# Kernel tuning notes

Measured on AMD Instinct MI355X. Metric: run time of the kernel, lower is better.

Reference implementation:

```python
import jax, jax.numpy as jnp
import numpy as np

TEMPERATURE = 1.0
TOP_K = 50
TOP_P = 0.95
NEG_INF = float('-inf')


def setup_inputs() -> dict:
    key = jax.random.key(0)
    k1, k2, k3, k4 = jax.random.split(key, 4)
    B, S, D, V = 32, 8, 1024, 50257
    psi_real = jax.random.normal(k1, (B, S, D), dtype=jnp.float32)
    psi_imag = jax.random.normal(k2, (B, S, D), dtype=jnp.float32)
    W_real = jax.random.normal(k3, (V, D), dtype=jnp.float32) * 0.02
    W_imag = jax.random.normal(k4, (V, D), dtype=jnp.float32) * 0.02
    bias = jnp.zeros((V,), dtype=jnp.float32)
    return {"psi_real": psi_real, "psi_imag": psi_imag, "W_real": W_real,
            "W_imag": W_imag, "bias": bias}


def _legacy_filter(logits, temperature, top_k, top_p):
    # temperature
    l = logits / max(temperature, 1e-8)
    # top-k: keep values >= k-th largest
    if 0 < top_k < l.shape[-1]:
        topk_vals = jax.lax.top_k(l, top_k)[0]          # [B,S,k]
        threshold = topk_vals[..., -1:]
        l = jnp.where(l < threshold, NEG_INF, l)
    # top-p (nucleus): mask tokens where exclusive cumulative prob >= p
    if top_p < 1.0:
        p = max(top_p, 1e-6)
        order = jnp.argsort(-l, axis=-1)                # descending
        sl = jnp.take_along_axis(l, order, axis=-1)
        sp = jax.nn.softmax(sl, axis=-1)
        cum = jnp.cumsum(sp, axis=-1)
        mask = (cum - sp) >= p                          # exclusive cumsum >= p
        mask = mask.at[..., 0].set(False)               # always keep top token
        sl = jnp.where(mask, NEG_INF, sl)
        inv = jnp.argsort(order, axis=-1)               # scatter back to original order
        l = jnp.take_along_axis(sl, inv, axis=-1)
    return l


def reference(psi_real, psi_imag, W_real, W_imag, bias):
    # logits = proj_real(psi.real) + proj_imag(psi.imag) + bias  -> [B,S,V]
    logits = (jnp.einsum('bsd,vd->bsv', psi_real, W_real)
              + jnp.einsum('bsd,vd->bsv', psi_imag, W_imag) + bias)
    sampling_logits = _legacy_filter(logits, TEMPERATURE, TOP_K, TOP_P)
    probs = jax.nn.softmax(sampling_logits, axis=-1)
    # multinomial(probs, 1) == categorical over filtered logits
    tokens = jax.random.categorical(jax.random.key(42), sampling_logits, axis=-1)
    log_probs = jax.nn.log_softmax(logits, axis=-1)
    return logits, tokens, probs, log_probs
```

## Files before the change

kernel.cpp:

```cpp
#include <hip/hip_runtime.h>
#include <stdint.h>
#include <math.h>

#define MM 256
#define KD 1024
#define K2 2048
#define VV 50257
#define NF4 (VV / 4)

static constexpr size_t OUT_TOKENS = (size_t)MM * VV;
static constexpr size_t OUT_PROBS  = OUT_TOKENS + MM;
static constexpr size_t OUT_LOGPR  = OUT_PROBS + (size_t)MM * VV;

#define WS_ABUF_BYTES (2u * 1024u * 1024u)

typedef __attribute__((ext_vector_type(8))) short bf16x8;
typedef __attribute__((ext_vector_type(4))) float f32x4;

__device__ __forceinline__ ushort f2bf(float x) {
  unsigned u = __float_as_uint(x);
  unsigned r = u + 0x7FFFu + ((u >> 16) & 1u);
  return (ushort)(r >> 16);
}
__device__ __forceinline__ float bf2f(ushort h) {
  return __uint_as_float(((unsigned)h) << 16);
}

__device__ __forceinline__ unsigned rotl32(unsigned x, int r) {
  return (x << r) | (x >> (32 - r));
}

__device__ __forceinline__ uint2 threefry2x32(unsigned k0, unsigned k1,
                                              unsigned x0, unsigned x1) {
  unsigned ks[3] = {k0, k1, k0 ^ k1 ^ 0x1BD11BDAu};
  const int rot[8] = {13, 15, 26, 6, 17, 29, 16, 24};
  x0 += ks[0]; x1 += ks[1];
  #pragma unroll
  for (int g = 0; g < 5; ++g) {
    const int base = (g & 1) ? 4 : 0;
    #pragma unroll
    for (int i = 0; i < 4; ++i) {
      x0 += x1;
      x1 = rotl32(x1, rot[base + i]);
      x1 ^= x0;
    }
    x0 += ks[(g + 1) % 3];
    x1 += ks[(g + 2) % 3] + (unsigned)(g + 1);
  }
  return make_uint2(x0, x1);
}

__device__ __forceinline__ float gumbel_at(unsigned flat) {
  uint2 r = threefry2x32(0u, 42u, 0u, flat);
  unsigned w = r.x ^ r.y;
  unsigned fb = (w >> 9) | 0x3F800000u;
  float f = __uint_as_float(fb) - 1.0f;
  const float tiny = 1.1754943508222875e-38f;
  float u = fmaxf(tiny, f + tiny);
  float t1 = (float)log((double)u);
  float t3 = (float)log((double)(-t1));
  return -t3;
}

__global__ __launch_bounds__(256)
void k_prep(const float* __restrict__ psi_r, const float* __restrict__ psi_i,
            ushort* __restrict__ a_buf) {
  int t = blockIdx.x * 256 + threadIdx.x;
  int lane = t & 63;
  int mb = (t >> 6) & 15;
  int s = t >> 10;
  int lr = lane & 15, lg = lane >> 4;
  int m = mb * 16 + lr;
  int kloc = (s & 31) * 32 + lg * 8;
  const float* __restrict__ src = (s < 32) ? psi_r : psi_i;
  float4 v0 = *reinterpret_cast<const float4*>(&src[m * KD + kloc]);
  float4 v1 = *reinterpret_cast<const float4*>(&src[m * KD + kloc + 4]);
  float in[8] = {v0.x, v0.y, v0.z, v0.w, v1.x, v1.y, v1.z, v1.w};
  ushort h[8], l[8];
  #pragma unroll
  for (int j = 0; j < 8; ++j) {
    h[j] = f2bf(in[j]);
    l[j] = f2bf(in[j] - bf2f(h[j]));
  }
  size_t base = ((size_t)(s * 16 + mb) * 2) * 512 + (size_t)lane * 8;
  #pragma unroll
  for (int j = 0; j < 8; ++j) {
    a_buf[base + j] = h[j];
    a_buf[base + 512 + j] = l[j];
  }
}

#define BN 64
#define BK 64
#define GT 256

__global__ __launch_bounds__(GT, 2)
void k_gemm(const uint4* __restrict__ a_buf,
            const float* __restrict__ Wr, const float* __restrict__ Wi,
            const float* __restrict__ bias, float* __restrict__ logits) {
  __shared__ ushort sBh[2][BN * BK];
  __shared__ ushort sBl[2][BN * BK];

  const int tid  = threadIdx.x;
  const int lane = tid & 63;
  const int wid  = tid >> 6;
  const int vb   = blockIdx.x * BN;
  const int lr = lane & 15;
  const int lg = lane >> 4;

  const int brow = tid >> 2;
  const int bcol = (tid & 3) << 4;
  const int gn   = vb + brow;
  const int eo0  = brow * BK + (bcol ^ ((brow & 7) << 3));
  const int eo1  = brow * BK + ((bcol + 8) ^ ((brow & 7) << 3));

  f32x4 acc[4][4];
  #pragma unroll
  for (int i = 0; i < 4; ++i)
    #pragma unroll
    for (int j = 0; j < 4; ++j)
      #pragma unroll
      for (int q = 0; q < 4; ++q) acc[i][j][q] = 0.f;

  float4 w0 = make_float4(0.f, 0.f, 0.f, 0.f), w1 = w0, w2 = w0, w3 = w0;
  if (gn < VV) {
    const float* p = &Wr[(size_t)gn * KD + bcol];
    w0 = *reinterpret_cast<const float4*>(p);
    w1 = *reinterpret_cast<const float4*>(p + 4);
    w2 = *reinterpret_cast<const float4*>(p + 8);
    w3 = *reinterpret_cast<const float4*>(p + 12);
  }

  int cur = 0;
  for (int s2 = 0; s2 < K2 / BK; ++s2) {
    uint4 vah[2][4], val[2][4];
    #pragma unroll
    for (int kq = 0; kq < 2; ++kq) {
      #pragma unroll
      for (int mi = 0; mi < 4; ++mi) {
        int chunk2 = (((s2 * 2 + kq) * 16) + wid * 4 + mi) * 2;
        vah[kq][mi] = a_buf[(size_t)chunk2 * 64 + lane];
        val[kq][mi] = a_buf[(size_t)(chunk2 + 1) * 64 + lane];
      }
    }
    {
      float in[16] = {w0.x, w0.y, w0.z, w0.w, w1.x, w1.y, w1.z, w1.w,
                      w2.x, w2.y, w2.z, w2.w, w3.x, w3.y, w3.z, w3.w};
      ushort h[16], l[16];
      #pragma unroll
      for (int j = 0; j < 16; ++j) {
        h[j] = f2bf(in[j]);
        l[j] = f2bf(in[j] - bf2f(h[j]));
      }
      *reinterpret_cast<uint4*>(&sBh[cur][eo0]) =
          make_uint4((unsigned)h[0] | ((unsigned)h[1] << 16),
                     (unsigned)h[2] | ((unsigned)h[3] << 16),
                     (unsigned)h[4] | ((unsigned)h[5] << 16),
                     (unsigned)h[6] | ((unsigned)h[7] << 16));
      *reinterpret_cast<uint4*>(&sBh[cur][eo1]) =
          make_uint4((unsigned)h[8] | ((unsigned)h[9] << 16),
                     (unsigned)h[10] | ((unsigned)h[11] << 16),
                     (unsigned)h[12] | ((unsigned)h[13] << 16),
                     (unsigned)h[14] | ((unsigned)h[15] << 16));
      *reinterpret_cast<uint4*>(&sBl[cur][eo0]) =
          make_uint4((unsigned)l[0] | ((unsigned)l[1] << 16),
                     (unsigned)l[2] | ((unsigned)l[3] << 16),
                     (unsigned)l[4] | ((unsigned)l[5] << 16),
                     (unsigned)l[6] | ((unsigned)l[7] << 16));
      *reinterpret_cast<uint4*>(&sBl[cur][eo1]) =
          make_uint4((unsigned)l[8] | ((unsigned)l[9] << 16),
                     (unsigned)l[10] | ((unsigned)l[11] << 16),
                     (unsigned)l[12] | ((unsigned)l[13] << 16),
                     (unsigned)l[14] | ((unsigned)l[15] << 16));
    }
    if (s2 < K2 / BK - 1) {
      int kk = (s2 + 1) * BK;
      const float* __restrict__ Bs = (kk < KD) ? Wr : Wi;
      int ko = kk & (KD - 1);
      if (gn < VV) {
        const float* p = &Bs[(size_t)gn * KD + ko + bcol];
        w0 = *reinterpret_cast<const float4*>(p);
        w1 = *reinterpret_cast<const float4*>(p + 4);
        w2 = *reinterpret_cast<const float4*>(p + 8);
        w3 = *reinterpret_cast<const float4*>(p + 12);
      }
    }
    asm volatile("s_waitcnt lgkmcnt(0)" ::: "memory");
    asm volatile("s_barrier" ::: "memory");

    #pragma unroll
    for (int kq = 0; kq < 2; ++kq) {
      bf16x8 bh[4], bl[4];
      #pragma unroll
      for (int ni = 0; ni < 4; ++ni) {
        int r = ni * 16 + lr;
        int eoff = r * BK + ((kq * 32 + lg * 8) ^ ((r & 7) << 3));
        bh[ni] = *reinterpret_cast<const bf16x8*>(&sBh[cur][eoff]);
        bl[ni] = *reinterpret_cast<const bf16x8*>(&sBl[cur][eoff]);
      }
      __builtin_amdgcn_s_setprio(1);
      #pragma unroll
      for (int mi = 0; mi < 4; ++mi) {
        bf16x8 ah = *reinterpret_cast<bf16x8*>(&vah[kq][mi]);
        bf16x8 al = *reinterpret_cast<bf16x8*>(&val[kq][mi]);
        #pragma unroll
        for (int ni = 0; ni < 4; ++ni) {
          acc[mi][ni] = __builtin_amdgcn_mfma_f32_16x16x32_bf16(ah, bh[ni], acc[mi][ni], 0, 0, 0);
          acc[mi][ni] = __builtin_amdgcn_mfma_f32_16x16x32_bf16(al, bh[ni], acc[mi][ni], 0, 0, 0);
          acc[mi][ni] = __builtin_amdgcn_mfma_f32_16x16x32_bf16(ah, bl[ni], acc[mi][ni], 0, 0, 0);
        }
      }
      __builtin_amdgcn_s_setprio(0);
    }
    cur ^= 1;
  }

  #pragma unroll
  for (int ni = 0; ni < 4; ++ni) {
    int n = vb + ni * 16 + lr;
    if (n < VV) {
      float b = bias[n];
      #pragma unroll
      for (int mi = 0; mi < 4; ++mi) {
        #pragma unroll
        for (int j = 0; j < 4; ++j) {
          int m = wid * 64 + mi * 16 + lg * 4 + j;
          logits[(size_t)m * VV + n] = acc[mi][ni][j] + b;
        }
      }
    }
  }
}

__device__ __forceinline__ unsigned ordf(float f) {
  unsigned u = __float_as_uint(f);
  return u ^ ((u >> 31) ? 0xFFFFFFFFu : 0x80000000u);
}

#define HREP 4
#define HSTRIDE 4097

__global__ __launch_bounds__(1024)
void k_stats(const float* __restrict__ logits, float* __restrict__ ws4) {
  const int row = blockIdx.x;
  const int tid = threadIdx.x;
  const float* __restrict__ x = logits + (size_t)row * VV;

  __shared__ unsigned hist[HREP * HSTRIDE];
  __shared__ float pm[16], ps[16];

  for (int i = tid; i < HREP * HSTRIDE; i += 1024) hist[i] = 0u;
  __syncthreads();

  const int rep = (tid & 3) * HSTRIDE;
  float lm = -INFINITY, ls = 0.f;
  for (int i4 = tid; i4 < NF4; i4 += 1024) {
    float4 v4 = *reinterpret_cast<const float4*>(&x[i4 * 4]);
    float vs[4] = {v4.x, v4.y, v4.z, v4.w};
    #pragma unroll
    for (int j = 0; j < 4; ++j) {
      float v = vs[j];
      atomicAdd(&hist[rep + (ordf(v) >> 20)], 1u);
      if (v <= lm) {
        ls += expf(v - lm);
      } else {
        ls = ls * expf(lm - v) + 1.f;
        lm = v;
      }
    }
  }
  if (tid == 0) {
    float v = x[VV - 1];
    atomicAdd(&hist[ordf(v) >> 20], 1u);
    if (v <= lm) ls += expf(v - lm);
    else { ls = ls * expf(lm - v) + 1.f; lm = v; }
  }
  #pragma unroll
  for (int off = 32; off; off >>= 1) {
    float om = __shfl_xor(lm, off);
    float os = __shfl_xor(ls, off);
    float M = fmaxf(lm, om);
    ls = ls * expf(lm - M) + os * expf(om - M);
    lm = M;
  }
  if ((tid & 63) == 0) { pm[tid >> 6] = lm; ps[tid >> 6] = ls; }
  __syncthreads();

  for (int b = tid; b < 4096; b += 1024)
    hist[b] = hist[b] + hist[HSTRIDE + b] + hist[2 * HSTRIDE + b] + hist[3 * HSTRIDE + b];
  __syncthreads();

  if (tid < 64) {
    float m2 = (tid < 16) ? pm[tid] : -3e38f;
    float s2 = (tid < 16) ? ps[tid] : 0.f;
    #pragma unroll
    for (int off = 8; off; off >>= 1) {
      float om = __shfl_xor(m2, off);
      float os = __shfl_xor(s2, off);
      float M = fmaxf(m2, om);
      s2 = s2 * expf(m2 - M) + os * expf(om - M);
      m2 = M;
    }
    unsigned seg = 0;
    #pragma unroll 8
    for (int b = 0; b < 64; ++b) seg += hist[tid * 64 + ((b + tid) & 63)];
    unsigned suf = seg;
    #pragma unroll
    for (int off = 1; off < 64; off <<= 1) {
      unsigned o = __shfl_down(suf, off);
      if (tid + off < 64) suf += o;
    }
    unsigned long long mk = __ballot(suf >= 50u);
    int lstar = 63 - __builtin_clzll(mk);
    unsigned above = (lstar < 63) ? (unsigned)__shfl((int)suf, lstar + 1) : 0u;
    if (tid == 0) {
      unsigned cum = above;
      int bin = lstar * 64;
      for (int b = 63; b >= 0; --b) {
        cum += hist[lstar * 64 + b];
        if (cum >= 50u) { bin = lstar * 64 + b; break; }
      }
      ws4[row * 4 + 0] = m2;
      ws4[row * 4 + 1] = logf(s2);
      ws4[row * 4 + 2] = __uint_as_float((unsigned)bin << 20);
    }
  }
}

#define CAP 1024

__global__ __launch_bounds__(1024)
void k_post(const float* __restrict__ logits, const float* __restrict__ ws4,
            float* __restrict__ logpr, float* __restrict__ probs,
            float* __restrict__ tokens) {
  const int row = blockIdx.x;
  const int tid = threadIdx.x;
  const float* __restrict__ x = logits + (size_t)row * VV;
  float* __restrict__ lp = logpr + (size_t)row * VV;
  float* __restrict__ pr = probs + (size_t)row * VV;

  __shared__ float cv[CAP];
  __shared__ int   ci[CAP];
  __shared__ unsigned s_cnt;
  __shared__ float top_v[50];
  __shared__ int   top_i[50];

  if (tid == 0) s_cnt = 0u;
  __syncthreads();

  const float mx = ws4[row * 4 + 0];
  const float lz = ws4[row * 4 + 1];
  const unsigned lo = __float_as_uint(ws4[row * 4 + 2]);
  const float4 z4 = make_float4(0.f, 0.f, 0.f, 0.f);

  for (int i4 = tid; i4 < NF4; i4 += 1024) {
    float4 v = *reinterpret_cast<const float4*>(&x[i4 * 4]);
    *reinterpret_cast<float4*>(&lp[i4 * 4]) =
        make_float4((v.x - mx) - lz, (v.y - mx) - lz,
                    (v.z - mx) - lz, (v.w - mx) - lz);
    *reinterpret_cast<float4*>(&pr[i4 * 4]) = z4;
    float vs[4] = {v.x, v.y, v.z, v.w};
    #pragma unroll
    for (int j = 0; j < 4; ++j) {
      if (ordf(vs[j]) >= lo) {
        unsigned pos = atomicAdd(&s_cnt, 1u);
        if (pos < CAP) { cv[pos] = vs[j]; ci[pos] = i4 * 4 + j; }
      }
    }
  }
  if (tid == 0) {
    float v = x[VV - 1];
    lp[VV - 1] = (v - mx) - lz;
    pr[VV - 1] = 0.f;
    if (ordf(v) >= lo) {
      unsigned pos = atomicAdd(&s_cnt, 1u);
      if (pos < CAP) { cv[pos] = v; ci[pos] = VV - 1; }
    }
  }
  __syncthreads();
  const int ncand = (int)min(s_cnt, (unsigned)CAP);

  if (tid < 64) {
    for (int it = 0; it < 50; ++it) {
      float bv = -INFINITY;
      int bi = 0x7FFFFFFF, bs = 0;
      for (int c = tid; c < ncand; c += 64) {
        float v = cv[c];
        int id = ci[c];
        if (v > bv || (v == bv && id < bi)) { bv = v; bi = id; bs = c; }
      }
      #pragma unroll
      for (int off = 32; off; off >>= 1) {
        float ov = __shfl_xor(bv, off);
        int oi = __shfl_xor(bi, off);
        int os = __shfl_xor(bs, off);
        if (ov > bv || (ov == bv && oi < bi)) { bv = ov; bi = oi; bs = os; }
      }
      if (tid == 0) {
        top_v[it] = bv;
        top_i[it] = bi;
        cv[bs] = -INFINITY;
      }
    }

    float tv = (tid < 50) ? top_v[tid] : -3e38f;
    float m0 = top_v[0];
    float sp = (tid < 50) ? expf(tv - m0) : 0.f;
    float Z = sp;
    #pragma unroll
    for (int off = 32; off; off >>= 1) Z += __shfl_xor(Z, off);
    float pref = sp;
    #pragma unroll
    for (int off = 1; off < 64; off <<= 1) {
      float o = __shfl_up(pref, off);
      if (tid >= off) pref += o;
    }
    float excl = (pref - sp) / Z;
    bool keep = (tid < 50) && ((tid == 0) || (excl < 0.95f));
    float spk = keep ? sp : 0.f;
    float Z2 = spk;
    #pragma unroll
    for (int off = 32; off; off >>= 1) Z2 += __shfl_xor(Z2, off);

    float bt = -3e38f;
    int bidx = 0x7FFFFFFF;
    if (keep) {
      int idx = top_i[tid];
      pr[idx] = sp / Z2;
      bt = tv + gumbel_at((unsigned)((size_t)row * VV + idx));
      bidx = idx;
    }
    #pragma unroll
    for (int off = 32; off; off >>= 1) {
      float ot = __shfl_xor(bt, off);
      int oi = __shfl_xor(bidx, off);
      if (ot > bt || (ot == bt && oi < bidx)) { bt = ot; bidx = oi; }
    }
    if (tid == 0) tokens[row] = (float)bidx;
  }
}

extern "C" void kernel_launch(void* const* d_in, const int* in_sizes, int n_in,
                              void* d_out, int out_size, void* d_ws, size_t ws_size,
                              hipStream_t stream) {
  const float* psi_r = (const float*)d_in[0];
  const float* psi_i = (const float*)d_in[1];
  const float* Wr    = (const float*)d_in[2];
  const float* Wi    = (const float*)d_in[3];
  const float* bias  = (const float*)d_in[4];
  float* out = (float*)d_out;

  ushort* a_buf = (ushort*)d_ws;
  float* ws4    = (float*)((char*)d_ws + WS_ABUF_BYTES);

  float* logits = out;
  float* tokens = out + OUT_TOKENS;
  float* probs  = out + OUT_PROBS;
  float* logpr  = out + OUT_LOGPR;

  k_prep<<<256, 256, 0, stream>>>(psi_r, psi_i, a_buf);
  const int nblk = (VV + BN - 1) / BN;
  k_gemm<<<nblk, GT, 0, stream>>>((const uint4*)a_buf, Wr, Wi, bias, logits);
  k_stats<<<MM, 1024, 0, stream>>>(logits, ws4);
  k_post<<<MM, 1024, 0, stream>>>(logits, ws4, logpr, probs, tokens);
}
```

Baseline: 285.6 us.

## Deepen GEMM software pipeline with two-stage W prefetch and split A loads

Restructures the k_gemm main loop into a manually unrolled pair of steps. W is now prefetched two stages ahead in two register sets, and A-fragment loads are split per k-quarter so they overlap with MFMA compute. The goal is to hide global-load latency behind the matrix math instead of stalling at each stage. In exchange it needs more registers, which may reduce occupancy at the launch bound of 2, and it adds more complex stage bookkeeping.

```diff
diff --git a/kernel.cpp b/kernel.cpp
--- a/kernel.cpp
+++ b/kernel.cpp
@@ -7,6 +7,7 @@
 #define K2 2048
 #define VV 50257
 #define NF4 (VV / 4)
+#define NSTEP 32
 
 static constexpr size_t OUT_TOKENS = (size_t)MM * VV;
 static constexpr size_t OUT_PROBS  = OUT_TOKENS + MM;
@@ -94,6 +95,92 @@
 #define BK 64
 #define GT 256
 
+struct W4 { float4 a, b, c, d; };
+struct A8 { uint4 h[4]; uint4 l[4]; };
+
+__device__ __forceinline__ void loadW(W4& w, const float* __restrict__ Wr,
+                                      const float* __restrict__ Wi,
+                                      int t, int gn, int bcol) {
+  const float* __restrict__ Bs = (t < 16) ? Wr : Wi;
+  int ko = (t << 6) & (KD - 1);
+  if (gn < VV) {
+    const float* p = &Bs[(size_t)gn * KD + ko + bcol];
+    w.a = *reinterpret_cast<const float4*>(p);
+    w.b = *reinterpret_cast<const float4*>(p + 4);
+    w.c = *reinterpret_cast<const float4*>(p + 8);
+    w.d = *reinterpret_cast<const float4*>(p + 12);
+  }
+}
+
+__device__ __forceinline__ void stageW(const W4& w, ushort* __restrict__ bh,
+                                       ushort* __restrict__ bl, int eo0, int eo1) {
+  float in[16] = {w.a.x, w.a.y, w.a.z, w.a.w, w.b.x, w.b.y, w.b.z, w.b.w,
+                  w.c.x, w.c.y, w.c.z, w.c.w, w.d.x, w.d.y, w.d.z, w.d.w};
+  ushort h[16], l[16];
+  #pragma unroll
+  for (int j = 0; j < 16; ++j) {
+    h[j] = f2bf(in[j]);
+    l[j] = f2bf(in[j] - bf2f(h[j]));
+  }
+  *reinterpret_cast<uint4*>(&bh[eo0]) =
+      make_uint4((unsigned)h[0] | ((unsigned)h[1] << 16),
+                 (unsigned)h[2] | ((unsigned)h[3] << 16),
+                 (unsigned)h[4] | ((unsigned)h[5] << 16),
+                 (unsigned)h[6] | ((unsigned)h[7] << 16));
+  *reinterpret_cast<uint4*>(&bh[eo1]) =
+      make_uint4((unsigned)h[8] | ((unsigned)h[9] << 16),
+                 (unsigned)h[10] | ((unsigned)h[11] << 16),
+                 (unsigned)h[12] | ((unsigned)h[13] << 16),
+                 (unsigned)h[14] | ((unsigned)h[15] << 16));
+  *reinterpret_cast<uint4*>(&bl[eo0]) =
+      make_uint4((unsigned)l[0] | ((unsigned)l[1] << 16),
+                 (unsigned)l[2] | ((unsigned)l[3] << 16),
+                 (unsigned)l[4] | ((unsigned)l[5] << 16),
+                 (unsigned)l[6] | ((unsigned)l[7] << 16));
+  *reinterpret_cast<uint4*>(&bl[eo1]) =
+      make_uint4((unsigned)l[8] | ((unsigned)l[9] << 16),
+                 (unsigned)l[10] | ((unsigned)l[11] << 16),
+                 (unsigned)l[12] | ((unsigned)l[13] << 16),
+                 (unsigned)l[14] | ((unsigned)l[15] << 16));
+}
+
+__device__ __forceinline__ void loadA(A8& A, const uint4* __restrict__ a_buf,
+                                      int s, int kq, int wid, int lane) {
+  #pragma unroll
+  for (int mi = 0; mi < 4; ++mi) {
+    int chunk2 = (((s * 2 + kq) * 16) + wid * 4 + mi) * 2;
+    A.h[mi] = a_buf[(size_t)chunk2 * 64 + lane];
+    A.l[mi] = a_buf[(size_t)(chunk2 + 1) * 64 + lane];
+  }
+}
+
+__device__ __forceinline__ void computeKQ(f32x4 (&acc)[4][4], const A8& A,
+                                          const ushort* __restrict__ bhp,
+                                          const ushort* __restrict__ blp,
+                                          int kq, int lr, int lg) {
+  bf16x8 bh[4], bl[4];
+  #pragma unroll
+  for (int ni = 0; ni < 4; ++ni) {
+    int r = ni * 16 + lr;
+    int eoff = r * BK + ((kq * 32 + lg * 8) ^ ((r & 7) << 3));
+    bh[ni] = *reinterpret_cast<const bf16x8*>(&bhp[eoff]);
+    bl[ni] = *reinterpret_cast<const bf16x8*>(&blp[eoff]);
+  }
+  __builtin_amdgcn_s_setprio(1);
+  #pragma unroll
+  for (int mi = 0; mi < 4; ++mi) {
+    bf16x8 ah = *reinterpret_cast<const bf16x8*>(&A.h[mi]);
+    bf16x8 al = *reinterpret_cast<const bf16x8*>(&A.l[mi]);
+    #pragma unroll
+    for (int ni = 0; ni < 4; ++ni) {
+      acc[mi][ni] = __builtin_amdgcn_mfma_f32_16x16x32_bf16(ah, bh[ni], acc[mi][ni], 0, 0, 0);
+      acc[mi][ni] = __builtin_amdgcn_mfma_f32_16x16x32_bf16(al, bh[ni], acc[mi][ni], 0, 0, 0);
+      acc[mi][ni] = __builtin_amdgcn_mfma_f32_16x16x32_bf16(ah, bl[ni], acc[mi][ni], 0, 0, 0);
+    }
+  }
+  __builtin_amdgcn_s_setprio(0);
+}
+
 __global__ __launch_bounds__(GT, 2)
 void k_gemm(const uint4* __restrict__ a_buf,
             const float* __restrict__ Wr, const float* __restrict__ Wi,
@@ -122,97 +209,37 @@
       #pragma unroll
       for (int q = 0; q < 4; ++q) acc[i][j][q] = 0.f;
 
-  float4 w0 = make_float4(0.f, 0.f, 0.f, 0.f), w1 = w0, w2 = w0, w3 = w0;
-  if (gn < VV) {
-    const float* p = &Wr[(size_t)gn * KD + bcol];
-    w0 = *reinterpret_cast<const float4*>(p);
-    w1 = *reinterpret_cast<const float4*>(p + 4);
-    w2 = *reinterpret_cast<const float4*>(p + 8);
-    w3 = *reinterpret_cast<const float4*>(p + 12);
-  }
-
-  int cur = 0;
-  for (int s2 = 0; s2 < K2 / BK; ++s2) {
-    uint4 vah[2][4], val[2][4];
-    #pragma unroll
-    for (int kq = 0; kq < 2; ++kq) {
-      #pragma unroll
-      for (int mi = 0; mi < 4; ++mi) {
-        int chunk2 = (((s2 * 2 + kq) * 16) + wid * 4 + mi) * 2;
-        vah[kq][mi] = a_buf[(size_t)chunk2 * 64 + lane];
-        val[kq][mi] = a_buf[(size_t)(chunk2 + 1) * 64 + lane];
-      }
-    }
-    {
-      float in[16] = {w0.x, w0.y, w0.z, w0.w, w1.x, w1.y, w1.z, w1.w,
-                      w2.x, w2.y, w2.z, w2.w, w3.x, w3.y, w3.z, w3.w};
-      ushort h[16], l[16];
-      #pragma unroll
-      for (int j = 0; j < 16; ++j) {
-        h[j] = f2bf(in[j]);
-        l[j] = f2bf(in[j] - bf2f(h[j]));
-      }
-      *reinterpret_cast<uint4*>(&sBh[cur][eo0]) =
-          make_uint4((unsigned)h[0] | ((unsigned)h[1] << 16),
-                     (unsigned)h[2] | ((unsigned)h[3] << 16),
-                     (unsigned)h[4] | ((unsigned)h[5] << 16),
-                     (unsigned)h[6] | ((unsigned)h[7] << 16));
-      *reinterpret_cast<uint4*>(&sBh[cur][eo1]) =
-          make_uint4((unsigned)h[8] | ((unsigned)h[9] << 16),
-                     (unsigned)h[10] | ((unsigned)h[11] << 16),
-                     (unsigned)h[12] | ((unsigned)h[13] << 16),
-                     (unsigned)h[14] | ((unsigned)h[15] << 16));
-      *reinterpret_cast<uint4*>(&sBl[cur][eo0]) =
-          make_uint4((unsigned)l[0] | ((unsigned)l[1] << 16),
-                     (unsigned)l[2] | ((unsigned)l[3] << 16),
-                     (unsigned)l[4] | ((unsigned)l[5] << 16),
-                     (unsigned)l[6] | ((unsigned)l[7] << 16));
-      *reinterpret_cast<uint4*>(&sBl[cur][eo1]) =
-          make_uint4((unsigned)l[8] | ((unsigned)l[9] << 16),
-                     (unsigned)l[10] | ((unsigned)l[11] << 16),
-                     (unsigned)l[12] | ((unsigned)l[13] << 16),
-                     (unsigned)l[14] | ((unsigned)l[15] << 16));
-    }
-    if (s2 < K2 / BK - 1) {
-      int kk = (s2 + 1) * BK;
-      const float* __restrict__ Bs = (kk < KD) ? Wr : Wi;
-      int ko = kk & (KD - 1);
-      if (gn < VV) {
-        const float* p = &Bs[(size_t)gn * KD + ko + bcol];
-        w0 = *reinterpret_cast<const float4*>(p);
-        w1 = *reinterpret_cast<const float4*>(p + 4);
-        w2 = *reinterpret_cast<const float4*>(p + 8);
-        w3 = *reinterpret_cast<const float4*>(p + 12);
-      }
-    }
+  W4 wX, wY;
+  wX.a = wX.b = wX.c = wX.d = make_float4(0.f, 0.f, 0.f, 0.f);
+  wY = wX;
+  A8 A0, A1;
+  loadW(wX, Wr, Wi, 0, gn, bcol);
+  loadW(wY, Wr, Wi, 1, gn, bcol);
+  loadA(A0, a_buf, 0, 0, wid, lane);
+  stageW(wX, &sBh[0][0], &sBl[0][0], eo0, eo1);
+  loadW(wX, Wr, Wi, 2, gn, bcol);
+  asm volatile("s_waitcnt lgkmcnt(0)" ::: "memory");
+  asm volatile("s_barrier" ::: "memory");
+
+  for (int sp = 0; sp < NSTEP / 2; ++sp) {
+    const int s0 = sp * 2;
+    const int s1 = s0 + 1;
+    loadA(A1, a_buf, s0, 1, wid, lane);
+    stageW(wY, &sBh[1][0], &sBl[1][0], eo0, eo1);
+    if (s0 + 3 < NSTEP) loadW(wY, Wr, Wi, s0 + 3, gn, bcol);
+    computeKQ(acc, A0, &sBh[0][0], &sBl[0][0], 0, lr, lg);
+    loadA(A0, a_buf, s1, 0, wid, lane);
+    computeKQ(acc, A1, &sBh[0][0], &sBl[0][0], 1, lr, lg);
     asm volatile("s_waitcnt lgkmcnt(0)" ::: "memory");
     asm volatile("s_barrier" ::: "memory");
-
-    #pragma unroll
-    for (int kq = 0; kq < 2; ++kq) {
-      bf16x8 bh[4], bl[4];
-      #pragma unroll
-      for (int ni = 0; ni < 4; ++ni) {
-        int r = ni * 16 + lr;
-        int eoff = r * BK + ((kq * 32 + lg * 8) ^ ((r & 7) << 3));
-        bh[ni] = *reinterpret_cast<const bf16x8*>(&sBh[cur][eoff]);
-        bl[ni] = *reinterpret_cast<const bf16x8*>(&sBl[cur][eoff]);
-      }
-      __builtin_amdgcn_s_setprio(1);
-      #pragma unroll
-      for (int mi = 0; mi < 4; ++mi) {
-        bf16x8 ah = *reinterpret_cast<bf16x8*>(&vah[kq][mi]);
-        bf16x8 al = *reinterpret_cast<bf16x8*>(&val[kq][mi]);
-        #pragma unroll
-        for (int ni = 0; ni < 4; ++ni) {
-          acc[mi][ni] = __builtin_amdgcn_mfma_f32_16x16x32_bf16(ah, bh[ni], acc[mi][ni], 0, 0, 0);
-          acc[mi][ni] = __builtin_amdgcn_mfma_f32_16x16x32_bf16(al, bh[ni], acc[mi][ni], 0, 0, 0);
-          acc[mi][ni] = __builtin_amdgcn_mfma_f32_16x16x32_bf16(ah, bl[ni], acc[mi][ni], 0, 0, 0);
-        }
-      }
-      __builtin_amdgcn_s_setprio(0);
-    }
-    cur ^= 1;
+    loadA(A1, a_buf, s1, 1, wid, lane);
+    if (s1 + 1 < NSTEP) stageW(wX, &sBh[0][0], &sBl[0][0], eo0, eo1);
+    if (s1 + 3 < NSTEP) loadW(wX, Wr, Wi, s1 + 3, gn, bcol);
+    computeKQ(acc, A0, &sBh[1][0], &sBl[1][0], 0, lr, lg);
+    if (s1 < NSTEP - 1) loadA(A0, a_buf, s1 + 1, 0, wid, lane);
+    computeKQ(acc, A1, &sBh[1][0], &sBl[1][0], 1, lr, lg);
+    asm volatile("s_waitcnt lgkmcnt(0)" ::: "memory");
+    asm volatile("s_barrier" ::: "memory");
   }
 
   #pragma unroll
```

New measurement: 284.1 us. Within noise of the previous version (-0.5%).
